# Optimization experiments

Hardware: AMD Instinct MI355X
Metric: run time of the kernel (lower is better)

## Reference

```python
import jax, jax.numpy as jnp
import numpy as np

# Per-channel class frequencies from the original module (23 AU channels)
_W = np.array([0.0012597430655963838, 0.0004919313290455535, 0.0021106513104319356,
               0.0007678117365508301, 0.004719881670572202, 0.000372272357115554,
               0.029090425620315438, 0.010056339432617042, 0.0034817436971298467,
               0.0003057951504877765, 0.003995280118329428, 8.808229878180519e-05,
               0.012070598793438699, 0.016788818533845208, 0.0017832510677901316,
               0.0008758371973209686, 0.0005933090691529143, 0.0031992155689617922,
               0.003212511010287348, 0.0016685778863572154, 0.0009356666832859684,
               0.0010985358395240233, 0.00103372056306194], dtype=np.float32)
_WEIGHT_0 = 1.0 / (_W + 1.0)        # used when target == 0
_WEIGHT_1 = 1.0 - _WEIGHT_0          # used when target == 1

B, C = 1000000, 23

def setup_inputs() -> dict:
    key = jax.random.key(0)
    k1, k2 = jax.random.split(key)
    # probabilities strictly inside (0,1) so log terms stay finite
    x = jax.random.uniform(k1, (B, C), dtype=jnp.float32) * 0.98 + 0.01
    labels = jax.random.randint(k2, (B, C), 0, 2, dtype=jnp.int32)
    return {"x": x, "labels": labels}

def reference(x, labels):
    # target = (labels > 0).float(); the eq(999) mask in the original is computed but unused
    target = (labels > 0).astype(x.dtype)
    w0 = jnp.asarray(_WEIGHT_0, dtype=x.dtype)  # [C]
    w1 = jnp.asarray(_WEIGHT_1, dtype=x.dtype)  # [C]
    # per-element weight: 1/weight_0[ch] if target==0 else 1/weight_1[ch]
    w = jnp.where(target == 0, 1.0 / w0, 1.0 / w1)  # [B, C] via broadcast
    bce = -(target * jnp.log(x) + (1.0 - target) * jnp.log(1.0 - x))
    loss = jnp.sum(w * bce)
    n, c = x.shape
    return loss / (n * c)
```

## Files before the change

kernel.cpp:

```cpp
#include <hip/hip_runtime.h>

#define NCH 23

__device__ __constant__ float d_W[NCH] = {
    0.0012597430655963838f, 0.0004919313290455535f, 0.0021106513104319356f,
    0.0007678117365508301f, 0.004719881670572202f,  0.000372272357115554f,
    0.029090425620315438f,  0.010056339432617042f,  0.0034817436971298467f,
    0.0003057951504877765f, 0.003995280118329428f,  8.808229878180519e-05f,
    0.012070598793438699f,  0.016788818533845208f,  0.0017832510677901316f,
    0.0008758371973209686f, 0.0005933090691529143f, 0.0031992155689617922f,
    0.003212511010287348f,  0.0016685778863572154f, 0.0009356666832859684f,
    0.0010985358395240233f, 0.00103372056306194f
};

__device__ __forceinline__ void accum_elem(float xx, int lab, unsigned c,
                                           const float* s_w0, const float* s_w1,
                                           float& acc) {
    bool t = lab > 0;
    float v = t ? xx : 1.0f - xx;
    float w = t ? s_w1[c] : s_w0[c];
    acc -= w * __logf(v);
}

__global__ __launch_bounds__(256) void bce_reduce_kernel(
        const float* __restrict__ x, const int* __restrict__ labels,
        double* __restrict__ partial, unsigned n ) {
    __shared__ float s_w0[NCH];
    __shared__ float s_w1[NCH];
    __shared__ float s_part[4];

    if (threadIdx.x < NCH) {
        float W  = d_W[threadIdx.x];
        float w0 = 1.0f / (W + 1.0f);
        float w1 = 1.0f - w0;
        s_w0[threadIdx.x] = 1.0f / w0;
        s_w1[threadIdx.x] = 1.0f / w1;
    }
    __syncthreads();

    const unsigned n4 = n >> 2;
    const unsigned stride = gridDim.x * blockDim.x;
    float acc = 0.0f;

    for (unsigned k = blockIdx.x * blockDim.x + threadIdx.x; k < n4; k += stride) {
        float4 xv = ((const float4*)x)[k];
        int4   lv = ((const int4*)labels)[k];
        unsigned c = (4u * k) % 23u;
        accum_elem(xv.x, lv.x, c, s_w0, s_w1, acc);  c = (c + 1u == 23u) ? 0u : c + 1u;
        accum_elem(xv.y, lv.y, c, s_w0, s_w1, acc);  c = (c + 1u == 23u) ? 0u : c + 1u;
        accum_elem(xv.z, lv.z, c, s_w0, s_w1, acc);  c = (c + 1u == 23u) ? 0u : c + 1u;
        accum_elem(xv.w, lv.w, c, s_w0, s_w1, acc);
    }

    unsigned tail_start = n4 << 2;
    for (unsigned i = tail_start + blockIdx.x * blockDim.x + threadIdx.x; i < n;
         i += stride) {
        accum_elem(x[i], labels[i], i % 23u, s_w0, s_w1, acc);
    }

    #pragma unroll
    for (int off = 32; off > 0; off >>= 1) acc += __shfl_down(acc, off, 64);
    int wave = threadIdx.x >> 6;
    int lane = threadIdx.x & 63;
    if (lane == 0) s_part[wave] = acc;
    __syncthreads();
    if (threadIdx.x == 0) {
        float s = s_part[0] + s_part[1] + s_part[2] + s_part[3];
        atomicAdd(partial, (double)s);
    }
}

__global__ void bce_finalize_kernel(const double* __restrict__ partial,
                                    float* __restrict__ out, unsigned n) {
    out[0] = (float)(partial[0] / (double)n);
}

extern "C" void kernel_launch(void* const* d_in, const int* in_sizes, int n_in,
                              void* d_out, int out_size, void* d_ws, size_t ws_size,
                              hipStream_t stream) {
    const float* x      = (const float*)d_in[0];
    const int*   labels = (const int*)d_in[1];
    float*       out    = (float*)d_out;
    double*      acc    = (double*)d_ws;
    unsigned n = (unsigned)in_sizes[0];

    hipMemsetAsync(acc, 0, sizeof(double), stream);

    const int block = 256;
    const int grid  = 2048;
    bce_reduce_kernel<<<grid, block, 0, stream>>>(x, labels, acc, n);
    bce_finalize_kernel<<<1, 1, 0, stream>>>(acc, out, n);
}
```

Baseline: 208.1 us.

## Process channel-aligned 92-element chunks per thread with compile-time weights

Each thread loads a contiguous chunk of 23 float4 values of x and labels. The chunk is a multiple of the channel count, so per-element channel weights become compile-time constants. The weights are pre-multiplied by -ln2 so log2 plus FMA replaces log, and the shared-memory weight table and its barrier are removed. The grid is sized to one chunk per thread instead of a grid-stride loop. This risks uncoalesced strided loads across threads, high register use and fewer blocks for latency hiding.

```diff
diff --git a/kernel.cpp b/kernel.cpp
--- a/kernel.cpp
+++ b/kernel.cpp
@@ -1,8 +1,11 @@
 #include <hip/hip_runtime.h>
+#include <utility>
 
 #define NCH 23
+#define CHUNK_V4 23
+#define CHUNK_ELEMS 92
 
-__device__ __constant__ float d_W[NCH] = {
+constexpr float c_W[NCH] = {
     0.0012597430655963838f, 0.0004919313290455535f, 0.0021106513104319356f,
     0.0007678117365508301f, 0.004719881670572202f,  0.000372272357115554f,
     0.029090425620315438f,  0.010056339432617042f,  0.0034817436971298467f,
@@ -12,56 +15,76 @@
     0.003212511010287348f,  0.0016685778863572154f, 0.0009356666832859684f,
     0.0010985358395240233f, 0.00103372056306194f
 };
+constexpr float NEG_LN2 = -0.69314718055994530942f;
 
-__device__ __forceinline__ void accum_elem(float xx, int lab, unsigned c,
-                                           const float* s_w0, const float* s_w1,
-                                           float& acc) {
-    bool t = lab > 0;
+struct Tabs { float w0n[NCH]; float w1n[NCH]; };
+
+constexpr Tabs make_tabs() {
+    Tabs t{};
+    for (int c = 0; c < NCH; ++c) {
+        float w0 = 1.0f / (c_W[c] + 1.0f);
+        float w1 = 1.0f - w0;
+        t.w0n[c] = (1.0f / w0) * NEG_LN2;
+        t.w1n[c] = (1.0f / w1) * NEG_LN2;
+    }
+    return t;
+}
+
+constexpr Tabs c_tabs = make_tabs();
+__constant__ Tabs d_tabs = make_tabs();
+
+__device__ __forceinline__ void elem(float xx, int lab, float w0n, float w1n,
+                                     float& acc) {
+    bool t  = lab > 0;
     float v = t ? xx : 1.0f - xx;
-    float w = t ? s_w1[c] : s_w0[c];
-    acc -= w * __logf(v);
+    float w = t ? w1n : w0n;
+    acc = __builtin_fmaf(w, __log2f(v), acc);
+}
+
+template <int J>
+__device__ __forceinline__ void do_vec4(const float4& xv, const int4& lv, float& acc) {
+    elem(xv.x, lv.x, c_tabs.w0n[(4 * J + 0) % NCH], c_tabs.w1n[(4 * J + 0) % NCH], acc);
+    elem(xv.y, lv.y, c_tabs.w0n[(4 * J + 1) % NCH], c_tabs.w1n[(4 * J + 1) % NCH], acc);
+    elem(xv.z, lv.z, c_tabs.w0n[(4 * J + 2) % NCH], c_tabs.w1n[(4 * J + 2) % NCH], acc);
+    elem(xv.w, lv.w, c_tabs.w0n[(4 * J + 3) % NCH], c_tabs.w1n[(4 * J + 3) % NCH], acc);
+}
+
+template <int... J>
+__device__ __forceinline__ void do_chunk(const float4* __restrict__ xp,
+                                         const int4* __restrict__ lp, float& acc,
+                                         std::integer_sequence<int, J...>) {
+    float4 xv[CHUNK_V4];
+    int4   lv[CHUNK_V4];
+    ((xv[J] = xp[J]), ...);
+    ((lv[J] = lp[J]), ...);
+    (do_vec4<J>(xv[J], lv[J], acc), ...);
 }
 
 __global__ __launch_bounds__(256) void bce_reduce_kernel(
         const float* __restrict__ x, const int* __restrict__ labels,
-        double* __restrict__ partial, unsigned n ) {
-    __shared__ float s_w0[NCH];
-    __shared__ float s_w1[NCH];
-    __shared__ float s_part[4];
-
-    if (threadIdx.x < NCH) {
-        float W  = d_W[threadIdx.x];
-        float w0 = 1.0f / (W + 1.0f);
-        float w1 = 1.0f - w0;
-        s_w0[threadIdx.x] = 1.0f / w0;
-        s_w1[threadIdx.x] = 1.0f / w1;
-    }
-    __syncthreads();
-
-    const unsigned n4 = n >> 2;
-    const unsigned stride = gridDim.x * blockDim.x;
+        double* __restrict__ partial, unsigned n) {
+    const unsigned nchunks = n / CHUNK_ELEMS;
+    const unsigned t = blockIdx.x * blockDim.x + threadIdx.x;
     float acc = 0.0f;
 
-    for (unsigned k = blockIdx.x * blockDim.x + threadIdx.x; k < n4; k += stride) {
-        float4 xv = ((const float4*)x)[k];
-        int4   lv = ((const int4*)labels)[k];
-        unsigned c = (4u * k) % 23u;
-        accum_elem(xv.x, lv.x, c, s_w0, s_w1, acc);  c = (c + 1u == 23u) ? 0u : c + 1u;
-        accum_elem(xv.y, lv.y, c, s_w0, s_w1, acc);  c = (c + 1u == 23u) ? 0u : c + 1u;
-        accum_elem(xv.z, lv.z, c, s_w0, s_w1, acc);  c = (c + 1u == 23u) ? 0u : c + 1u;
-        accum_elem(xv.w, lv.w, c, s_w0, s_w1, acc);
+    if (t < nchunks) {
+        const float4* xp = (const float4*)x + (size_t)t * CHUNK_V4;
+        const int4*   lp = (const int4*)labels + (size_t)t * CHUNK_V4;
+        do_chunk(xp, lp, acc, std::make_integer_sequence<int, CHUNK_V4>{});
     }
 
-    unsigned tail_start = n4 << 2;
-    for (unsigned i = tail_start + blockIdx.x * blockDim.x + threadIdx.x; i < n;
-         i += stride) {
-        accum_elem(x[i], labels[i], i % 23u, s_w0, s_w1, acc);
+    const unsigned tail = nchunks * CHUNK_ELEMS;
+    const unsigned nthreads = gridDim.x * blockDim.x;
+    for (unsigned i = tail + t; i < n; i += nthreads) {
+        unsigned c = i % NCH;
+        elem(x[i], labels[i], d_tabs.w0n[c], d_tabs.w1n[c], acc);
     }
 
     #pragma unroll
     for (int off = 32; off > 0; off >>= 1) acc += __shfl_down(acc, off, 64);
-    int wave = threadIdx.x >> 6;
-    int lane = threadIdx.x & 63;
+    __shared__ float s_part[4];
+    const int wave = threadIdx.x >> 6;
+    const int lane = threadIdx.x & 63;
     if (lane == 0) s_part[wave] = acc;
     __syncthreads();
     if (threadIdx.x == 0) {
@@ -86,8 +109,9 @@
 
     hipMemsetAsync(acc, 0, sizeof(double), stream);
 
+    const unsigned nchunks = n / CHUNK_ELEMS;
     const int block = 256;
-    const int grid  = 2048;
+    const int grid  = (int)((nchunks + block - 1) / block);
     bce_reduce_kernel<<<grid, block, 0, stream>>>(x, labels, acc, n);
     bce_finalize_kernel<<<1, 1, 0, stream>>>(acc, out, n);
 }
```

Result: slower. 230.6 us (+10.8%).
